# Kernel tuning notes

Measured on AMD Instinct MI355X. Metric: run time of the kernel, lower is better.

The kernel has to match this reference:

```python
import jax, jax.numpy as jnp
import numpy as np
import math

B, T, IN_DIM, HID = 64, 512, 1024, 1024
TAU_MEM = 20.0
ALPHA = math.exp(-1.0 / TAU_MEM)
THRESHOLD = 1.0


def setup_inputs() -> dict:
    key = jax.random.key(0)
    kx, kw, kb = jax.random.split(key, 3)
    s = 1.0 / math.sqrt(IN_DIM)  # torch Linear default init scale
    x = jax.random.normal(kx, (B, T, IN_DIM), dtype=jnp.float32)
    W = jax.random.uniform(kw, (HID, IN_DIM), minval=-s, maxval=s, dtype=jnp.float32)
    b = jax.random.uniform(kb, (HID,), minval=-s, maxval=s, dtype=jnp.float32)
    return {"x": x, "W": W, "b": b}


def reference(x, W, b):
    # Precompute the batched GEMM once: I[b,t,h] = fc(x[:,t])
    I = jnp.einsum("bti,hi->bth", x, W) + b  # [B,T,H]

    def step(mem, I_t):
        mem = ALPHA * mem + I_t                         # leaky integrate
        spike = (mem >= THRESHOLD).astype(mem.dtype)    # fire
        mem = mem * (1.0 - spike)                       # hard reset
        return mem, spike

    mem0 = jnp.zeros((x.shape[0], HID), dtype=x.dtype)
    mem_final, spikes_tbh = jax.lax.scan(step, mem0, jnp.swapaxes(I, 0, 1))
    spikes = jnp.swapaxes(spikes_tbh, 0, 1)  # [B,T,H]
    return spikes, mem_final
```

## Files before the change

### kernel.cpp

```cpp
#include <hip/hip_runtime.h>

#define B_    64
#define T_    512
#define KDIM  1024
#define HID_  1024

#define BM 64
#define BN 64
#define BK 32
#define LDA 36
#define NSLICE ((T_ / BM) * (KDIM / BK))

#define ALPHA_F 0.95122942450071400909f

typedef float v4f __attribute__((ext_vector_type(4)));
typedef float v2f __attribute__((ext_vector_type(2)));

__global__ __launch_bounds__(256, 2) void snn_np_pf(
    const float* __restrict__ x,
    const float* __restrict__ W,
    const float* __restrict__ bias,
    float* __restrict__ spikes,
    float* __restrict__ memf)
{
#pragma clang fp contract(off)
    __shared__ float As[BM][LDA];
    __shared__ float Bs[BN][LDA];
    __shared__ float Ism[BM][BN + 1];
    __shared__ float bsh[BN];

    const int tid = threadIdx.x;
    const int bb  = blockIdx.x;
    const int h0  = blockIdx.y * BN;

    const int tx = tid & 15;
    const int ty = tid >> 4;

    const int sr0 = tid >> 3;
    const int sr1 = 32 + sr0;
    const int sc  = (tid & 7) << 2;

    const float* xb = x + (size_t)bb * T_ * KDIM;
    const float* Wb = W + (size_t)h0 * KDIM;

    if (tid < BN) bsh[tid] = bias[h0 + tid];

    float mem = 0.0f;

    float4 pa0 = *(const float4*)&xb[(size_t)sr0 * KDIM + sc];
    float4 pa1 = *(const float4*)&xb[(size_t)sr1 * KDIM + sc];
    float4 pw0 = *(const float4*)&Wb[(size_t)sr0 * KDIM + sc];
    float4 pw1 = *(const float4*)&Wb[(size_t)sr1 * KDIM + sc];

    for (int c = 0; c < T_ / BM; ++c) {
        const int t0 = c * BM;
        v2f p01[4][4], p23[4][4];
#pragma unroll
        for (int j = 0; j < 4; ++j)
#pragma unroll
            for (int i = 0; i < 4; ++i) {
                p01[j][i] = (v2f)(0.0f);
                p23[j][i] = (v2f)(0.0f);
            }

        for (int s = 0; s < KDIM / BK; ++s) {
            __syncthreads();
            *(float4*)&As[sr0][sc] = pa0;
            *(float4*)&As[sr1][sc] = pa1;
            *(float4*)&Bs[sr0][sc] = pw0;
            *(float4*)&Bs[sr1][sc] = pw1;
            const int g1 = c * (KDIM / BK) + s + 1;
            if (g1 < NSLICE) {
                const int nt0 = (g1 >> 5) * BM;
                const int nk  = (g1 & 31) << 5;
                pa0 = *(const float4*)&xb[(size_t)(nt0 + sr0) * KDIM + nk + sc];
                pa1 = *(const float4*)&xb[(size_t)(nt0 + sr1) * KDIM + nk + sc];
                pw0 = *(const float4*)&Wb[(size_t)sr0 * KDIM + nk + sc];
                pw1 = *(const float4*)&Wb[(size_t)sr1 * KDIM + nk + sc];
            }
            __syncthreads();
#pragma unroll
            for (int kb = 0; kb < 2; ++kb) {
#pragma unroll
                for (int q = 3; q >= 0; --q) {
                    const int qc = (kb << 4) + (q << 2);
                    v2f a01[4], a23[4], b01[4], b23[4];
#pragma unroll
                    for (int j = 0; j < 4; ++j) {
                        const v4f a = *(const v4f*)&As[ty + 16 * j][qc];
                        a01[j] = a.xy; a23[j] = a.zw;
                    }
#pragma unroll
                    for (int i = 0; i < 4; ++i) {
                        const v4f b = *(const v4f*)&Bs[tx + 16 * i][qc];
                        b01[i] = b.xy; b23[i] = b.zw;
                    }
#pragma unroll
                    for (int j = 0; j < 4; ++j)
#pragma unroll
                        for (int i = 0; i < 4; ++i) {
                            const v2f m01 = a01[j] * b01[i];
                            const v2f m23 = a23[j] * b23[i];
                            p01[j][i] = p01[j][i] + m01;
                            p23[j][i] = p23[j][i] + m23;
                        }
                }
            }
        }

#pragma unroll
        for (int j = 0; j < 4; ++j)
#pragma unroll
            for (int i = 0; i < 4; ++i) {
                const float s01 = p01[j][i].x + p01[j][i].y;
                const float s23 = p23[j][i].x + p23[j][i].y;
                Ism[ty + 16 * j][tx + 16 * i] = (s01 + s23) + bsh[tx + 16 * i];
            }
        __syncthreads();

        if (tid < BN) {
            const size_t srow0 = ((size_t)(bb * T_ + t0)) * HID_ + h0 + tid;
#pragma unroll 4
            for (int t = 0; t < BM; ++t) {
                const float It = Ism[t][tid];
                const float am = ALPHA_F * mem;
                mem = am + It;
                const bool fire = (mem >= 1.0f);
                spikes[srow0 + (size_t)t * HID_] = fire ? 1.0f : 0.0f;
                if (fire) mem = 0.0f;
            }
        }
    }

    if (tid < BN) memf[(size_t)bb * HID_ + h0 + tid] = mem;
}

extern "C" void kernel_launch(void* const* d_in, const int* in_sizes, int n_in,
                              void* d_out, int out_size, void* d_ws, size_t ws_size,
                              hipStream_t stream) {
    const float* x    = (const float*)d_in[0];
    const float* W    = (const float*)d_in[1];
    const float* bias = (const float*)d_in[2];
    float* out    = (float*)d_out;
    float* spikes = out;
    float* memf   = out + (size_t)B_ * T_ * HID_;

    dim3 grid(B_, HID_ / BN);
    snn_np_pf<<<grid, dim3(256), 0, stream>>>(x, W, bias, spikes, memf);
}
```

Baseline: 1.505 ms.

## Double-buffer LDS tiles to use one barrier per k-slice

```diff
diff --git a/kernel.cpp b/kernel.cpp
--- a/kernel.cpp
+++ b/kernel.cpp
@@ -9,14 +9,16 @@
 #define BN 64
 #define BK 32
 #define LDA 36
-#define NSLICE ((T_ / BM) * (KDIM / BK))
+#define NSL 256
+#define SPC 32
+#define BOFF 2304
 
 #define ALPHA_F 0.95122942450071400909f
 
 typedef float v4f __attribute__((ext_vector_type(4)));
 typedef float v2f __attribute__((ext_vector_type(2)));
 
-__global__ __launch_bounds__(256, 2) void snn_np_pf(
+__global__ __launch_bounds__(256, 2) void snn_np_db(
     const float* __restrict__ x,
     const float* __restrict__ W,
     const float* __restrict__ bias,
@@ -24,10 +26,11 @@
     float* __restrict__ memf)
 {
 #pragma clang fp contract(off)
-    __shared__ float As[BM][LDA];
-    __shared__ float Bs[BN][LDA];
-    __shared__ float Ism[BM][BN + 1];
-    __shared__ float bsh[BN];
+    __shared__ float smem[9280];
+    float* const AB0 = smem;
+    float* const AB1 = smem + 4608;
+    float* const Ism = smem + 4608;
+    float* const bsh = smem + 9216;
 
     const int tid = threadIdx.x;
     const int bb  = blockIdx.x;
@@ -47,13 +50,22 @@
 
     float mem = 0.0f;
 
-    float4 pa0 = *(const float4*)&xb[(size_t)sr0 * KDIM + sc];
-    float4 pa1 = *(const float4*)&xb[(size_t)sr1 * KDIM + sc];
-    float4 pw0 = *(const float4*)&Wb[(size_t)sr0 * KDIM + sc];
-    float4 pw1 = *(const float4*)&Wb[(size_t)sr1 * KDIM + sc];
+    float4 pa0, pa1, pw0, pw1;
+    pa0 = *(const float4*)&xb[(size_t)sr0 * KDIM + sc];
+    pa1 = *(const float4*)&xb[(size_t)sr1 * KDIM + sc];
+    pw0 = *(const float4*)&Wb[(size_t)sr0 * KDIM + sc];
+    pw1 = *(const float4*)&Wb[(size_t)sr1 * KDIM + sc];
+    *(float4*)&AB0[sr0 * LDA + sc]        = pa0;
+    *(float4*)&AB0[sr1 * LDA + sc]        = pa1;
+    *(float4*)&AB0[BOFF + sr0 * LDA + sc] = pw0;
+    *(float4*)&AB0[BOFF + sr1 * LDA + sc] = pw1;
+    pa0 = *(const float4*)&xb[(size_t)sr0 * KDIM + 32 + sc];
+    pa1 = *(const float4*)&xb[(size_t)sr1 * KDIM + 32 + sc];
+    pw0 = *(const float4*)&Wb[(size_t)sr0 * KDIM + 32 + sc];
+    pw1 = *(const float4*)&Wb[(size_t)sr1 * KDIM + 32 + sc];
+    __syncthreads();
 
     for (int c = 0; c < T_ / BM; ++c) {
-        const int t0 = c * BM;
         v2f p01[4][4], p23[4][4];
 #pragma unroll
         for (int j = 0; j < 4; ++j)
@@ -63,22 +75,26 @@
                 p23[j][i] = (v2f)(0.0f);
             }
 
-        for (int s = 0; s < KDIM / BK; ++s) {
-            __syncthreads();
-            *(float4*)&As[sr0][sc] = pa0;
-            *(float4*)&As[sr1][sc] = pa1;
-            *(float4*)&Bs[sr0][sc] = pw0;
-            *(float4*)&Bs[sr1][sc] = pw1;
-            const int g1 = c * (KDIM / BK) + s + 1;
-            if (g1 < NSLICE) {
-                const int nt0 = (g1 >> 5) * BM;
-                const int nk  = (g1 & 31) << 5;
+        for (int s = 0; s < SPC; ++s) {
+            const int g = c * SPC + s;
+            float* const cb = (g & 1) ? AB1 : AB0;
+            float* const nb = (g & 1) ? AB0 : AB1;
+
+            if (g + 1 < NSL) {
+                *(float4*)&nb[sr0 * LDA + sc]        = pa0;
+                *(float4*)&nb[sr1 * LDA + sc]        = pa1;
+                *(float4*)&nb[BOFF + sr0 * LDA + sc] = pw0;
+                *(float4*)&nb[BOFF + sr1 * LDA + sc] = pw1;
+            }
+            if (g + 2 < NSL) {
+                const int gs  = g + 2;
+                const int nt0 = (gs >> 5) * BM;
+                const int nk  = (gs & 31) << 5;
                 pa0 = *(const float4*)&xb[(size_t)(nt0 + sr0) * KDIM + nk + sc];
                 pa1 = *(const float4*)&xb[(size_t)(nt0 + sr1) * KDIM + nk + sc];
                 pw0 = *(const float4*)&Wb[(size_t)sr0 * KDIM + nk + sc];
                 pw1 = *(const float4*)&Wb[(size_t)sr1 * KDIM + nk + sc];
             }
-            __syncthreads();
 #pragma unroll
             for (int kb = 0; kb < 2; ++kb) {
 #pragma unroll
@@ -87,12 +103,12 @@
                     v2f a01[4], a23[4], b01[4], b23[4];
 #pragma unroll
                     for (int j = 0; j < 4; ++j) {
-                        const v4f a = *(const v4f*)&As[ty + 16 * j][qc];
+                        const v4f a = *(const v4f*)&cb[(ty + 16 * j) * LDA + qc];
                         a01[j] = a.xy; a23[j] = a.zw;
                     }
 #pragma unroll
                     for (int i = 0; i < 4; ++i) {
-                        const v4f b = *(const v4f*)&Bs[tx + 16 * i][qc];
+                        const v4f b = *(const v4f*)&cb[BOFF + (tx + 16 * i) * LDA + qc];
                         b01[i] = b.xy; b23[i] = b.zw;
                     }
 #pragma unroll
@@ -106,6 +122,7 @@
                         }
                 }
             }
+            __syncthreads();
         }
 
 #pragma unroll
@@ -114,15 +131,16 @@
             for (int i = 0; i < 4; ++i) {
                 const float s01 = p01[j][i].x + p01[j][i].y;
                 const float s23 = p23[j][i].x + p23[j][i].y;
-                Ism[ty + 16 * j][tx + 16 * i] = (s01 + s23) + bsh[tx + 16 * i];
+                Ism[(ty + 16 * j) * (BN + 1) + (tx + 16 * i)] =
+                    (s01 + s23) + bsh[tx + 16 * i];
             }
         __syncthreads();
 
         if (tid < BN) {
-            const size_t srow0 = ((size_t)(bb * T_ + t0)) * HID_ + h0 + tid;
+            const size_t srow0 = ((size_t)(bb * T_ + c * BM)) * HID_ + h0 + tid;
 #pragma unroll 4
             for (int t = 0; t < BM; ++t) {
-                const float It = Ism[t][tid];
+                const float It = Ism[t * (BN + 1) + tid];
                 const float am = ALPHA_F * mem;
                 mem = am + It;
                 const bool fire = (mem >= 1.0f);
@@ -130,6 +148,7 @@
                 if (fire) mem = 0.0f;
             }
         }
+        __syncthreads();
     }
 
     if (tid < BN) memf[(size_t)bb * HID_ + h0 + tid] = mem;
@@ -146,5 +165,5 @@
     float* memf   = out + (size_t)B_ * T_ * HID_;
 
     dim3 grid(B_, HID_ / BN);
-    snn_np_pf<<<grid, dim3(256), 0, stream>>>(x, W, bias, spikes, memf);
+    snn_np_db<<<grid, dim3(256), 0, stream>>>(x, W, bias, spikes, memf);
 }
```

Measured after the change: 1.500 ms. No clear change (-0.3%).

## Split K lanes across two thread halves with 8x4 micro-tiles and LDS reduction

Applied to the files above, without the earlier changes.

```diff
diff --git a/kernel.cpp b/kernel.cpp
--- a/kernel.cpp
+++ b/kernel.cpp
@@ -9,14 +9,15 @@
 #define BN 64
 #define BK 32
 #define LDA 36
-#define NSLICE ((T_ / BM) * (KDIM / BK))
+#define NSL 256
+#define SPC 32
 
 #define ALPHA_F 0.95122942450071400909f
 
 typedef float v4f __attribute__((ext_vector_type(4)));
 typedef float v2f __attribute__((ext_vector_type(2)));
 
-__global__ __launch_bounds__(256, 2) void snn_np_pf(
+__global__ __launch_bounds__(256, 2) void snn_np_ls(
     const float* __restrict__ x,
     const float* __restrict__ W,
     const float* __restrict__ bias,
@@ -24,17 +25,18 @@
     float* __restrict__ memf)
 {
 #pragma clang fp contract(off)
-    __shared__ float As[BM][LDA];
-    __shared__ float Bs[BN][LDA];
-    __shared__ float Ism[BM][BN + 1];
+    __shared__ float As[BM * LDA];
+    __shared__ float Bs[BN * LDA];
+    __shared__ float Ism[BM * (BN + 1)];
     __shared__ float bsh[BN];
 
     const int tid = threadIdx.x;
     const int bb  = blockIdx.x;
     const int h0  = blockIdx.y * BN;
 
-    const int tx = tid & 15;
-    const int ty = tid >> 4;
+    const int tx   = tid & 15;
+    const int ry   = (tid >> 4) & 7;
+    const int half = tid >> 7;
 
     const int sr0 = tid >> 3;
     const int sr1 = 32 + sr0;
@@ -53,24 +55,20 @@
     float4 pw1 = *(const float4*)&Wb[(size_t)sr1 * KDIM + sc];
 
     for (int c = 0; c < T_ / BM; ++c) {
-        const int t0 = c * BM;
-        v2f p01[4][4], p23[4][4];
+        v2f p[8][4];
 #pragma unroll
-        for (int j = 0; j < 4; ++j)
+        for (int j = 0; j < 8; ++j)
 #pragma unroll
-            for (int i = 0; i < 4; ++i) {
-                p01[j][i] = (v2f)(0.0f);
-                p23[j][i] = (v2f)(0.0f);
-            }
+            for (int i = 0; i < 4; ++i) p[j][i] = (v2f)(0.0f);
 
-        for (int s = 0; s < KDIM / BK; ++s) {
+        for (int s = 0; s < SPC; ++s) {
             __syncthreads();
-            *(float4*)&As[sr0][sc] = pa0;
-            *(float4*)&As[sr1][sc] = pa1;
-            *(float4*)&Bs[sr0][sc] = pw0;
-            *(float4*)&Bs[sr1][sc] = pw1;
-            const int g1 = c * (KDIM / BK) + s + 1;
-            if (g1 < NSLICE) {
+            *(float4*)&As[sr0 * LDA + sc] = pa0;
+            *(float4*)&As[sr1 * LDA + sc] = pa1;
+            *(float4*)&Bs[sr0 * LDA + sc] = pw0;
+            *(float4*)&Bs[sr1 * LDA + sc] = pw1;
+            const int g1 = c * SPC + s + 1;
+            if (g1 < NSL) {
                 const int nt0 = (g1 >> 5) * BM;
                 const int nk  = (g1 & 31) << 5;
                 pa0 = *(const float4*)&xb[(size_t)(nt0 + sr0) * KDIM + nk + sc];
@@ -83,46 +81,52 @@
             for (int kb = 0; kb < 2; ++kb) {
 #pragma unroll
                 for (int q = 3; q >= 0; --q) {
-                    const int qc = (kb << 4) + (q << 2);
-                    v2f a01[4], a23[4], b01[4], b23[4];
+                    const int qc = (kb << 4) + (q << 2) + (half << 1);
+                    v2f a2[8], b2[4];
 #pragma unroll
-                    for (int j = 0; j < 4; ++j) {
-                        const v4f a = *(const v4f*)&As[ty + 16 * j][qc];
-                        a01[j] = a.xy; a23[j] = a.zw;
-                    }
+                    for (int j = 0; j < 8; ++j)
+                        a2[j] = *(const v2f*)&As[(ry + 8 * j) * LDA + qc];
 #pragma unroll
-                    for (int i = 0; i < 4; ++i) {
-                        const v4f b = *(const v4f*)&Bs[tx + 16 * i][qc];
-                        b01[i] = b.xy; b23[i] = b.zw;
-                    }
+                    for (int i = 0; i < 4; ++i)
+                        b2[i] = *(const v2f*)&Bs[(tx + 16 * i) * LDA + qc];
 #pragma unroll
-                    for (int j = 0; j < 4; ++j)
+                    for (int j = 0; j < 8; ++j)
 #pragma unroll
                         for (int i = 0; i < 4; ++i) {
-                            const v2f m01 = a01[j] * b01[i];
-                            const v2f m23 = a23[j] * b23[i];
-                            p01[j][i] = p01[j][i] + m01;
-                            p23[j][i] = p23[j][i] + m23;
+                            const v2f m = a2[j] * b2[i];
+                            p[j][i] = p[j][i] + m;
                         }
                 }
             }
         }
 
+        if (half) {
 #pragma unroll
-        for (int j = 0; j < 4; ++j)
+            for (int j = 0; j < 8; ++j)
 #pragma unroll
-            for (int i = 0; i < 4; ++i) {
-                const float s01 = p01[j][i].x + p01[j][i].y;
-                const float s23 = p23[j][i].x + p23[j][i].y;
-                Ism[ty + 16 * j][tx + 16 * i] = (s01 + s23) + bsh[tx + 16 * i];
-            }
+                for (int i = 0; i < 4; ++i)
+                    Ism[(ry + 8 * j) * (BN + 1) + tx + 16 * i] =
+                        p[j][i].x + p[j][i].y;
+        }
+        __syncthreads();
+        if (!half) {
+#pragma unroll
+            for (int j = 0; j < 8; ++j)
+#pragma unroll
+                for (int i = 0; i < 4; ++i) {
+                    const int cell = (ry + 8 * j) * (BN + 1) + tx + 16 * i;
+                    const float s01 = p[j][i].x + p[j][i].y;
+                    const float s23 = Ism[cell];
+                    Ism[cell] = (s01 + s23) + bsh[tx + 16 * i];
+                }
+        }
         __syncthreads();
 
         if (tid < BN) {
-            const size_t srow0 = ((size_t)(bb * T_ + t0)) * HID_ + h0 + tid;
+            const size_t srow0 = ((size_t)(bb * T_ + c * BM)) * HID_ + h0 + tid;
 #pragma unroll 4
             for (int t = 0; t < BM; ++t) {
-                const float It = Ism[t][tid];
+                const float It = Ism[t * (BN + 1) + tid];
                 const float am = ALPHA_F * mem;
                 mem = am + It;
                 const bool fire = (mem >= 1.0f);
@@ -146,5 +150,5 @@
     float* memf   = out + (size_t)B_ * T_ * HID_;
 
     dim3 grid(B_, HID_ / BN);
-    snn_np_pf<<<grid, dim3(256), 0, stream>>>(x, W, bias, spikes, memf);
+    snn_np_ls<<<grid, dim3(256), 0, stream>>>(x, W, bias, spikes, memf);
 }
```

After: 1.689 ms. 12.2% more time.
